# Performance work log

Measured on AMD Instinct MI355X. Metric: run time of the kernel, lower is better.

## Reference

```python
import jax, jax.numpy as jnp
import numpy as np

LN_EPS = 1e-5
LOCAL_SIZE = 256
N_HEAD, D_HEAD = 16, 64


def layer_norm_c(x):
    # layer norm over channel dim (axis=1), no affine params (matches F.layer_norm(x.T,(d,)).T)
    m = jnp.mean(x, axis=1, keepdims=True)
    v = jnp.var(x, axis=1, keepdims=True)
    return (x - m) / jnp.sqrt(v + LN_EPS)


def rel_shift(x):
    # x: [b, n, q, k] -> Transformer-XL relative shift
    b, n, q, k = x.shape
    x = jnp.pad(x, ((0, 0), (0, 0), (0, 0), (1, 0)))
    return x.reshape(b, n, k + 1, q)[:, :, 1:].reshape(b, n, q, k)


def setup_inputs() -> dict:
    key = jax.random.key(0)
    ks = jax.random.split(key, 14)
    bsz, d_model, qlen, mlen = 4, 1024, 512, 512
    klen = qlen + mlen
    d_inner = 4096
    s = lambda k, shape, sc=0.05: jax.random.normal(k, shape, dtype=jnp.float32) * sc
    return {
        "z1ss": jax.random.normal(ks[0], (bsz, d_model, qlen), dtype=jnp.float32),
        "uss": jax.random.normal(ks[1], (bsz, 3 * d_model, klen), dtype=jnp.float32) * 0.1,
        "z0": jax.random.normal(ks[2], (bsz, d_model, mlen), dtype=jnp.float32),
        "pos_emb": jax.random.normal(ks[3], (1, d_model, klen), dtype=jnp.float32),
        "qkv_w": s(ks[4], (3 * d_model, d_model)),
        "r_w": s(ks[5], (d_model, d_model)),
        "r_w_bias": s(ks[6], (N_HEAD, D_HEAD)),
        "r_r_bias": s(ks[7], (N_HEAD, D_HEAD)),
        "o_w": s(ks[8], (d_model, d_model)),
        "o_b": s(ks[9], (d_model,)),
        "ff1_w": s(ks[10], (d_inner, d_model)),
        "ff1_b": s(ks[11], (d_inner,)),
        "ff2_w": s(ks[12], (d_model, d_inner)),
        "ff2_b": s(ks[13], (d_model,)),
    }


def reference(z1ss, uss, z0, pos_emb, qkv_w, r_w, r_w_bias, r_r_bias, o_w, o_b,
              ff1_w, ff1_b, ff2_w, ff2_b):
    bsz, d_model, qlen = z1ss.shape
    mlen = z0.shape[2]
    n_head, d_head = N_HEAD, D_HEAD
    scale = 1.0 / d_head ** 0.5

    # ---- self-attention (post-lnorm path) ----
    cat = jnp.concatenate([z0, z1ss], axis=-1)              # [b, d, klen]
    klen = cat.shape[2]
    w_heads = jnp.einsum('od,bdk->bok', qkv_w, cat) + uss   # [b, 3d, klen]
    r_head_k = jnp.einsum('od,dk->ok', r_w, pos_emb[0])     # [d, rlen]
    rlen = r_head_k.shape[1]

    w_head_q, w_head_k, w_head_v = jnp.split(w_heads, 3, axis=1)
    w_head_q = w_head_q[:, :, -qlen:]
    w_head_q = w_head_q.reshape(bsz, n_head, d_head, qlen)
    w_head_k = w_head_k.reshape(bsz, n_head, d_head, klen)
    w_head_v = w_head_v.reshape(bsz, n_head, d_head, klen)
    r_head_k = r_head_k.reshape(n_head, d_head, rlen)

    rw_q = w_head_q + r_w_bias[:, :, None]                  # [b,n,d,q]
    AC = jnp.einsum('bndi,bndj->bnij', rw_q, w_head_k)      # [b,n,q,k]
    rr_q = w_head_q + r_r_bias[:, :, None]
    BD = rel_shift(jnp.einsum('bndi,ndj->bnij', rr_q, r_head_k))
    attn_score = (AC + BD) * scale

    local_size = LOCAL_SIZE if LOCAL_SIZE else 1000
    i = jnp.arange(qlen)[:, None]
    j = jnp.arange(klen)[None, :]
    mask = (j > i + mlen) | (j <= i + mlen - local_size)    # causal + local window
    attn_score = jnp.where(mask[None, None], -jnp.inf, attn_score)

    attn_prob = jax.nn.softmax(attn_score, axis=-1)
    attn_vec = jnp.einsum('bnij,bndj->bndi', attn_prob, w_head_v)
    attn_vec = attn_vec.reshape(bsz, n_head * d_head, qlen)
    attn_out = jnp.einsum('od,bdq->boq', o_w, attn_vec) + o_b[None, :, None]
    x = layer_norm_c(attn_out + z1ss)                       # post-lnorm

    # ---- position-wise FF (weight-shared, post-lnorm) ----
    h = jax.nn.relu(jnp.einsum('id,bdq->biq', ff1_w, x) + ff1_b[None, :, None])
    out2 = jnp.einsum('di,biq->bdq', ff2_w, h) + ff2_b[None, :, None]
    return layer_norm_c(out2 + x)
```

## Files before the change

kernel.cpp:

```cpp
#include <hip/hip_runtime.h>
#include <hip/hip_bf16.h>

typedef unsigned short u16;
typedef __attribute__((ext_vector_type(8))) short s8v;
typedef __attribute__((ext_vector_type(4))) short s4v;
typedef __attribute__((ext_vector_type(4))) float f4v;

__device__ __forceinline__ float s2f(u16 s) {
    unsigned int u = ((unsigned int)s) << 16;
    return __builtin_bit_cast(float, u);
}
__device__ __forceinline__ u16 f2s(float f) {
    __hip_bfloat16 h = __float2bfloat16(f);
    return __builtin_bit_cast(u16, h);
}

__device__ __forceinline__ void gl2lds16(const u16* g, u16* l) {
    __builtin_amdgcn_global_load_lds((const __attribute__((address_space(1))) void*)g,
                                     (__attribute__((address_space(3))) void*)l, 16, 0, 0);
}

#define BSZ 4
#define DM 1024
#define QLEN 512
#define MLEN 512
#define KLEN 1024
#define DI 4096
#define NH 16
#define DH 64
#define WIN 256

__global__ __launch_bounds__(256) void conv_w5(
    const float* __restrict__ s0, const float* __restrict__ s1,
    const float* __restrict__ s2, const float* __restrict__ s3,
    const float* __restrict__ s4,
    u16* __restrict__ d0, u16* __restrict__ d1, u16* __restrict__ d2,
    u16* __restrict__ d3, u16* __restrict__ d4)
{
    const int e0 = 786432, e1 = e0 + 262144, e2 = e1 + 262144,
              e3 = e2 + 1048576, e4 = e3 + 1048576;
    int i = blockIdx.x * 256 + threadIdx.x;
    const float* s; u16* d; int off;
    if (i < e0)      { s = s0; d = d0; off = i; }
    else if (i < e1) { s = s1; d = d1; off = i - e0; }
    else if (i < e2) { s = s2; d = d2; off = i - e1; }
    else if (i < e3) { s = s3; d = d3; off = i - e2; }
    else if (i < e4) { s = s4; d = d4; off = i - e3; }
    else return;
    f4v v = *(const f4v*)&s[(size_t)off * 4];
    s4v o;
#pragma unroll
    for (int k = 0; k < 4; ++k) o[k] = (short)f2s(v[k]);
    *(s4v*)&d[(size_t)off * 4] = o;
}

__global__ __launch_bounds__(256) void trans_f2b(
    const float* __restrict__ src, long sS, int ldS, int colOff,
    u16* __restrict__ dst, long sD, int ldD, int rowOff)
{
    __shared__ float tile[32][33];
    int b = blockIdx.z;
    int t0 = blockIdx.x * 32, f0 = blockIdx.y * 32;
    int tx = threadIdx.x, ty = threadIdx.y;
#pragma unroll
    for (int p = 0; p < 4; ++p)
        tile[ty + 8 * p][tx] = src[(size_t)b * sS + (size_t)(f0 + ty + 8 * p) * ldS + colOff + t0 + tx];
    __syncthreads();
#pragma unroll
    for (int p = 0; p < 4; ++p)
        dst[(size_t)b * sD + (size_t)(rowOff + t0 + ty + 8 * p) * ldD + f0 + tx] = f2s(tile[tx][ty + 8 * p]);
}

__global__ __launch_bounds__(256) void trans_add(
    const float* __restrict__ src, u16* __restrict__ dst)
{
    __shared__ float tile[32][33];
    int b = blockIdx.z;
    int t0 = blockIdx.x * 32, f0 = blockIdx.y * 32;
    int tx = threadIdx.x, ty = threadIdx.y;
    const float* S = src + (size_t)b * 3072 * 1024;
    u16* D = dst + (size_t)b * 1024 * 3072;
#pragma unroll
    for (int p = 0; p < 4; ++p)
        tile[ty + 8 * p][tx] = S[(size_t)(f0 + ty + 8 * p) * 1024 + t0 + tx];
    __syncthreads();
#pragma unroll
    for (int p = 0; p < 4; ++p) {
        size_t o = (size_t)(t0 + ty + 8 * p) * 3072 + f0 + tx;
        D[o] = f2s(s2f(D[o]) + tile[tx][ty + 8 * p]);
    }
}

__global__ __launch_bounds__(256) void trans_b2f(
    const u16* __restrict__ src, long sS, int ldS,
    float* __restrict__ dst, long sD, int ldD)
{
    __shared__ float tile[32][33];
    int b = blockIdx.z;
    int t0 = blockIdx.x * 32, f0 = blockIdx.y * 32;
    int tx = threadIdx.x, ty = threadIdx.y;
#pragma unroll
    for (int p = 0; p < 4; ++p)
        tile[ty + 8 * p][tx] = s2f(src[(size_t)b * sS + (size_t)(f0 + ty + 8 * p) * ldS + t0 + tx]);
    __syncthreads();
#pragma unroll
    for (int p = 0; p < 4; ++p)
        dst[(size_t)b * sD + (size_t)(t0 + ty + 8 * p) * ldD + f0 + tx] = tile[tx][ty + 8 * p];
}

template<int BN, int SPLIT>
__global__ __launch_bounds__(256) void gemm_bt(
    const u16* __restrict__ A,
    const u16* __restrict__ B,
    u16* __restrict__ C,
    float* __restrict__ fOut,
    int M, int K,
    const float* __restrict__ bias,
    const float* __restrict__ uss,
    int relu,
    long pstride)
{
    constexpr int BM = 128, BK = 64;
    constexpr int MI = (BN == 128) ? 4 : 2;
    constexpr int NI = 4;
    const int n0 = blockIdx.x * BN, m0 = blockIdx.y * BM;
    const int Ks = K / SPLIT;
    const int kbeg = blockIdx.z * Ks;
    __shared__ __align__(16) u16 As[BM * BK];
    __shared__ __align__(16) u16 Bs[BN * BK];
    const int tid = threadIdx.x, lane = tid & 63, wv = tid >> 6;
    const int l15 = lane & 15, quad = lane >> 4;
    const int wm = (BN == 128) ? (wv >> 1) * 64 : wv * 32;
    const int wn = (BN == 128) ? (wv & 1) * 64 : 0;
    f4v acc[MI][NI] = {};
    for (int kk = kbeg; kk < kbeg + Ks; kk += BK) {
        __syncthreads();
#pragma unroll
        for (int p = 0; p < (BM * 8) / 256; ++p) {
            int c = p * 256 + tid, r = c >> 3, q = c & 7, qs = q ^ (r & 7);
            gl2lds16(&A[(size_t)(m0 + r) * K + kk + qs * 8], &As[c * 8]);
        }
#pragma unroll
        for (int p = 0; p < (BN * 8) / 256; ++p) {
            int c = p * 256 + tid, r = c >> 3, q = c & 7, qs = q ^ (r & 7);
            gl2lds16(&B[(size_t)(n0 + r) * K + kk + qs * 8], &Bs[c * 8]);
        }
        __syncthreads();
#pragma unroll
        for (int k0 = 0; k0 < BK; k0 += 32) {
            s8v af[MI], bf[NI];
#pragma unroll
            for (int mi = 0; mi < MI; ++mi) {
                int r = wm + mi * 16 + l15;
                af[mi] = *(const s8v*)&As[r * BK + ((((k0 >> 3) + quad) ^ (r & 7)) << 3)];
            }
#pragma unroll
            for (int ni = 0; ni < NI; ++ni) {
                int r = wn + ni * 16 + l15;
                bf[ni] = *(const s8v*)&Bs[r * BK + ((((k0 >> 3) + quad) ^ (r & 7)) << 3)];
            }
#pragma unroll
            for (int mi = 0; mi < MI; ++mi)
#pragma unroll
                for (int ni = 0; ni < NI; ++ni)
                    acc[mi][ni] = __builtin_amdgcn_mfma_f32_16x16x32_bf16(af[mi], bf[ni], acc[mi][ni], 0, 0, 0);
        }
    }
    if (SPLIT > 1) {
        float* base = fOut + (long)blockIdx.z * pstride;
#pragma unroll
        for (int mi = 0; mi < MI; ++mi) {
            int m = m0 + wm + mi * 16 + quad * 4;
#pragma unroll
            for (int ni = 0; ni < NI; ++ni) {
                int n = n0 + wn + ni * 16 + l15;
                *(f4v*)&base[(size_t)n * M + m] = acc[mi][ni];
            }
        }
    } else {
#pragma unroll
        for (int mi = 0; mi < MI; ++mi) {
            int m = m0 + wm + mi * 16 + quad * 4;
            float bv[4] = {0.f, 0.f, 0.f, 0.f};
            if (bias) {
#pragma unroll
                for (int r2 = 0; r2 < 4; ++r2) bv[r2] = bias[m + r2];
            }
#pragma unroll
            for (int ni = 0; ni < NI; ++ni) {
                int n = n0 + wn + ni * 16 + l15;
                float o[4];
#pragma unroll
                for (int r2 = 0; r2 < 4; ++r2) o[r2] = acc[mi][ni][r2] + bv[r2];
                if (uss) {
                    int b = n >> 10, t = n & 1023;
#pragma unroll
                    for (int r2 = 0; r2 < 4; ++r2)
                        o[r2] += uss[((size_t)b * 3072 + m + r2) * 1024 + t];
                }
                if (relu) {
#pragma unroll
                    for (int r2 = 0; r2 < 4; ++r2) o[r2] = fmaxf(o[r2], 0.f);
                }
                s4v st;
#pragma unroll
                for (int r2 = 0; r2 < 4; ++r2) st[r2] = (short)f2s(o[r2]);
                *(s4v*)&C[(size_t)n * M + m] = st;
            }
        }
    }
}

#define QT 16
#define KT 272
#define KROW 72
#define VROW 280
#define SROW 272
#define PROW 280
__global__ __launch_bounds__(256) void attn_mfma(
    const u16* __restrict__ WHT,
    const u16* __restrict__ RT,
    const float* __restrict__ rwb, const float* __restrict__ rrb,
    u16* __restrict__ avT)
{
    __shared__ __align__(16) u16  sKV[KT * KROW];
    __shared__ __align__(16) float sS[QT * SROW];
    __shared__ __align__(16) u16  sP[QT * PROW];

    const int qt = blockIdx.x, n = blockIdx.y, b = blockIdx.z;
    const int i0 = qt * QT, j0 = i0 + WIN + 1;
    const int tid = threadIdx.x, lane = tid & 63, wv = tid >> 6;
    const int l15 = lane & 15, quad = lane >> 4;
    const u16* W = WHT + (size_t)b * KLEN * (3 * DM);

    s8v qac[2], qbd[2];
    {
        int qrow = MLEN + i0 + l15;
#pragma unroll
        for (int kc = 0; kc < 2; ++kc) {
            int col = n * DH + kc * 32 + quad * 8;
            s8v qv = *(const s8v*)&W[(size_t)qrow * (3 * DM) + col];
            s8v a, c;
#pragma unroll
            for (int e = 0; e < 8; ++e) {
                float qf = s2f((u16)qv[e]);
                a[e] = (short)f2s(qf + rwb[col + e]);
                c[e] = (short)f2s(qf + rrb[col + e]);
            }
            qac[kc] = a; qbd[kc] = c;
        }
    }

    for (int t = tid; t < KT * 8; t += 256) {
        int r = t >> 3, q = t & 7;
        int j = j0 + r; if (j > KLEN - 1) j = KLEN - 1;
        *(s8v*)&sKV[r * KROW + q * 8] = *(const s8v*)&W[(size_t)j * (3 * DM) + DM + n * DH + q * 8];
    }
    for (int t = tid; t < QT * SROW; t += 256) sS[t] = -1e30f;
    __syncthreads();

#pragma unroll
    for (int cc = 0; cc < 4; ++cc) {
        int ci = wv + cc * 4;
        f4v acc = {};
#pragma unroll
        for (int kc = 0; kc < 2; ++kc) {
            s8v bf = *(const s8v*)&RT[(size_t)(ci * 16 + l15) * DM + n * DH + kc * 32 + quad * 8];
            acc = __builtin_amdgcn_mfma_f32_16x16x32_bf16(qbd[kc], bf, acc, 0, 0, 0);
        }
#pragma unroll
        for (int r2 = 0; r2 < 4; ++r2) {
            int qi = quad * 4 + r2;
            sS[qi * SROW + qi + ci * 16 + l15] = acc[r2];
        }
    }
    __syncthreads();

    for (int ci = wv; ci < 17; ci += 4) {
        f4v acc = {};
#pragma unroll
        for (int kc = 0; kc < 2; ++kc) {
            s8v bf = *(const s8v*)&sKV[(ci * 16 + l15) * KROW + kc * 32 + quad * 8];
            acc = __builtin_amdgcn_mfma_f32_16x16x32_bf16(qac[kc], bf, acc, 0, 0, 0);
        }
#pragma unroll
        for (int r2 = 0; r2 < 4; ++r2) {
            int qi = quad * 4 + r2;
            sS[qi * SROW + ci * 16 + l15] += acc[r2];
        }
    }
    __syncthreads();

    {
        int q = tid >> 5, r0 = tid & 31;
        for (int k = 0; k < 9; ++k) {
            int r = r0 + 32 * k;
            if (r < KT) {
                int j = j0 + r; if (j > KLEN - 1) j = KLEN - 1;
                s8v vv = *(const s8v*)&W[(size_t)j * (3 * DM) + 2 * DM + n * DH + q * 8];
#pragma unroll
                for (int e = 0; e < 8; ++e)
                    sKV[(q * 8 + e) * VROW + r] = (u16)vv[e];
            }
        }
    }

    {
        int g = tid >> 4, l = tid & 15;
        float vals[17], mx = -1e30f;
#pragma unroll
        for (int k = 0; k < 17; ++k) {
            float s = sS[g * SROW + l + 16 * k] * 0.125f;
            vals[k] = s; mx = fmaxf(mx, s);
        }
#pragma unroll
        for (int d = 1; d < 16; d <<= 1) mx = fmaxf(mx, __shfl_xor(mx, d, 16));
        float sum = 0.f;
#pragma unroll
        for (int k = 0; k < 17; ++k) { vals[k] = __expf(vals[k] - mx); sum += vals[k]; }
#pragma unroll
        for (int d = 1; d < 16; d <<= 1) sum += __shfl_xor(sum, d, 16);
        float inv = 1.f / sum;
#pragma unroll
        for (int k = 0; k < 17; ++k) sP[g * PROW + l + 16 * k] = f2s(vals[k] * inv);
    }
    __syncthreads();

    f4v o = {};
    for (int kc = 0; kc < 9; ++kc) {
        s8v a = {}, bb = {};
        if (kc < 8) {
            a  = *(const s8v*)&sP[l15 * PROW + kc * 32 + quad * 8];
            bb = *(const s8v*)&sKV[(wv * 16 + l15) * VROW + kc * 32 + quad * 8];
        } else if (quad < 2) {
            a  = *(const s8v*)&sP[l15 * PROW + 256 + quad * 8];
            bb = *(const s8v*)&sKV[(wv * 16 + l15) * VROW + 256 + quad * 8];
        }
        o = __builtin_amdgcn_mfma_f32_16x16x32_bf16(a, bb, o, 0, 0, 0);
    }
#pragma unroll
    for (int r2 = 0; r2 < 4; ++r2) {
        int qi = quad * 4 + r2;
        avT[((size_t)b * QLEN + i0 + qi) * DM + n * DH + wv * 16 + l15] = f2s(o[r2]);
    }
}

__global__ __launch_bounds__(256) void ln_f(
    const float* __restrict__ P, long pstride, int nparts,
    const float* __restrict__ bias,
    const u16* __restrict__ res, int resMode, u16* __restrict__ out)
{
    int n = blockIdx.x, tid = threadIdx.x;
    int lane = tid & 63, wv = tid >> 6;
    int f = tid * 4;
    int rrow = resMode ? (((n >> 9) * 2 + 1) * 512 + (n & 511)) : n;
    f4v pv = *(const f4v*)&P[(size_t)n * DM + f];
    for (int p = 1; p < nparts; ++p) {
        const float* Pp = P + (long)p * pstride;
        pv += *(const f4v*)&Pp[(size_t)n * DM + f];
    }
    s4v rv = *(const s4v*)&res[(size_t)rrow * DM + f];
    f4v bv = *(const f4v*)&bias[f];
    float v[4];
#pragma unroll
    for (int k = 0; k < 4; ++k) v[k] = pv[k] + bv[k] + s2f((u16)rv[k]);
    float s = v[0] + v[1] + v[2] + v[3];
    float ss = v[0] * v[0] + v[1] * v[1] + v[2] * v[2] + v[3] * v[3];
#pragma unroll
    for (int d = 1; d < 64; d <<= 1) {
        s += __shfl_xor(s, d, 64);
        ss += __shfl_xor(ss, d, 64);
    }
    __shared__ float ps[4], pss[4];
    if (lane == 0) { ps[wv] = s; pss[wv] = ss; }
    __syncthreads();
    float S = ps[0] + ps[1] + ps[2] + ps[3];
    float SS = pss[0] + pss[1] + pss[2] + pss[3];
    float m = S * (1.f / DM);
    float var = SS * (1.f / DM) - m * m;
    float inv = rsqrtf(fmaxf(var, 0.f) + 1e-5f);
    s4v st;
#pragma unroll
    for (int k = 0; k < 4; ++k) st[k] = (short)f2s((v[k] - m) * inv);
    *(s4v*)&out[(size_t)n * DM + f] = st;
}

extern "C" void kernel_launch(void* const* d_in, const int* in_sizes, int n_in,
                              void* d_out, int out_size, void* d_ws, size_t ws_size,
                              hipStream_t stream) {
    const float* z1ss  = (const float*)d_in[0];
    const float* uss   = (const float*)d_in[1];
    const float* z0    = (const float*)d_in[2];
    const float* pos   = (const float*)d_in[3];
    const float* qkv_w = (const float*)d_in[4];
    const float* r_w   = (const float*)d_in[5];
    const float* rwb   = (const float*)d_in[6];
    const float* rrb   = (const float*)d_in[7];
    const float* o_w   = (const float*)d_in[8];
    const float* o_b   = (const float*)d_in[9];
    const float* ff1_w = (const float*)d_in[10];
    const float* ff1_b = (const float*)d_in[11];
    const float* ff2_w = (const float*)d_in[12];
    const float* ff2_b = (const float*)d_in[13];

    u16* ws = (u16*)d_ws;
    u16* wQ   = ws;
    u16* wR   = ws + 3145728;
    u16* wO   = ws + 4194304;
    u16* wF1  = ws + 5242880;
    u16* wF2  = ws + 9437184;
    u16* catT = ws + 13631488;
    u16* whT  = ws + 17825792;
    u16* posT = ws + 30408704;
    u16* rT   = ws + 30670848;
    u16* avT  = ws + 30932992;
    u16* xT   = ws + 33030144;
    float* pref = (float*)(ws + 35127296);
    u16* hT   = whT;
    u16* outT = catT;

    float* part1 = (float*)d_ws;
    long pstr = part1 - pref;

    dim3 tblk(32, 8);

    conv_w5<<<13312, 256, 0, stream>>>(qkv_w, r_w, o_w, ff1_w, ff2_w,
                                       wQ, wR, wO, wF1, wF2);

    trans_f2b<<<dim3(16, 32, BSZ), tblk, 0, stream>>>(z0, (long)DM * MLEN, MLEN, 0,
                                                      catT, (long)KLEN * DM, DM, 0);
    trans_f2b<<<dim3(16, 32, BSZ), tblk, 0, stream>>>(z1ss, (long)DM * QLEN, QLEN, 0,
                                                      catT, (long)KLEN * DM, DM, MLEN);
    trans_f2b<<<dim3(8, 32, 1), tblk, 0, stream>>>(pos, 0, KLEN, KLEN - WIN,
                                                   posT, 0, DM, 0);

    gemm_bt<64, 1><<<dim3(64, 24, 1), 256, 0, stream>>>(
        wQ, catT, whT, nullptr, 3 * DM, DM, nullptr, nullptr, 0, 0);

    trans_add<<<dim3(32, 96, BSZ), tblk, 0, stream>>>(uss, whT);

    gemm_bt<64, 1><<<dim3(4, 8, 1), 256, 0, stream>>>(
        wR, posT, rT, nullptr, DM, DM, nullptr, nullptr, 0, 0);

    attn_mfma<<<dim3(QLEN / QT, NH, BSZ), 256, 0, stream>>>(whT, rT, rwb, rrb, avT);

    gemm_bt<64, 2><<<dim3(32, 8, 2), 256, 0, stream>>>(
        wO, avT, nullptr, pref, DM, DM, nullptr, nullptr, 0, pstr);

    ln_f<<<2048, 256, 0, stream>>>(pref, pstr, 2, o_b, catT, 1, xT);

    gemm_bt<64, 1><<<dim3(32, 32, 1), 256, 0, stream>>>(
        wF1, xT, hT, nullptr, DI, DM, ff1_b, nullptr, 1, 0);

    gemm_bt<64, 2><<<dim3(32, 8, 2), 256, 0, stream>>>(
        wF2, hT, nullptr, pref, DM, DI, nullptr, nullptr, 0, pstr);

    ln_f<<<2048, 256, 0, stream>>>(pref, pstr, 2, ff2_b, xT, 0, outT);

    trans_b2f<<<dim3(32, 16, BSZ), tblk, 0, stream>>>(outT, (long)QLEN * DM, DM,
                                                      (float*)d_out, (long)DM * QLEN, QLEN);
}
```

Baseline: 365.1 us.

## Emit transposed V from QKV GEMM and stream K/V directly in attention

The QKV GEMM epilogue now adds uss to the V rows and writes V transposed (feature-major) into a separate buffer, so the transpose-add kernel only processes Q and K. The attention kernel drops its shared-memory K and V staging. It reads K and V fragments straight from global memory and applies the relative shift when storing scores, which cuts the score buffer to 256 columns. Probabilities are packed as bf16 into the score buffer, shared memory use shrinks, and launch bounds request 4 blocks per CU for more occupancy. The cost is scattered uncoalesced 2-byte stores in the GEMM epilogue and more uncached global loads in attention.

```diff
diff --git a/kernel.cpp b/kernel.cpp
--- a/kernel.cpp
+++ b/kernel.cpp
@@ -116,9 +116,10 @@
     float* __restrict__ fOut,
     int M, int K,
     const float* __restrict__ bias,
-    const float* __restrict__ uss,
     int relu,
-    long pstride)
+    long pstride,
+    const float* __restrict__ ussV,
+    u16* __restrict__ vTout)
 {
     constexpr int BM = 128, BK = 64;
     constexpr int MI = (BN == 128) ? 4 : 2;
@@ -177,6 +178,21 @@
                 *(f4v*)&base[(size_t)n * M + m] = acc[mi][ni];
             }
         }
+    } else if (vTout && m0 >= 2048) {
+#pragma unroll
+        for (int mi = 0; mi < MI; ++mi) {
+            int m = m0 + wm + mi * 16 + quad * 4;
+#pragma unroll
+            for (int ni = 0; ni < NI; ++ni) {
+                int n = n0 + wn + ni * 16 + l15;
+                int b = n >> 10, t = n & 1023;
+#pragma unroll
+                for (int r2 = 0; r2 < 4; ++r2) {
+                    float o = acc[mi][ni][r2] + ussV[((size_t)b * 3072 + (m + r2)) * 1024 + t];
+                    vTout[(size_t)(m + r2 - 2048) * 4096 + n] = f2s(o);
+                }
+            }
+        }
     } else {
 #pragma unroll
         for (int mi = 0; mi < MI; ++mi) {
@@ -192,12 +208,6 @@
                 float o[4];
 #pragma unroll
                 for (int r2 = 0; r2 < 4; ++r2) o[r2] = acc[mi][ni][r2] + bv[r2];
-                if (uss) {
-                    int b = n >> 10, t = n & 1023;
-#pragma unroll
-                    for (int r2 = 0; r2 < 4; ++r2)
-                        o[r2] += uss[((size_t)b * 3072 + m + r2) * 1024 + t];
-                }
                 if (relu) {
 #pragma unroll
                     for (int r2 = 0; r2 < 4; ++r2) o[r2] = fmaxf(o[r2], 0.f);
@@ -212,20 +222,15 @@
 }
 
 #define QT 16
-#define KT 272
-#define KROW 72
-#define VROW 280
-#define SROW 272
-#define PROW 280
-__global__ __launch_bounds__(256) void attn_mfma(
+#define SROW 260
+__global__ __launch_bounds__(256, 4) void attn_mfma(
     const u16* __restrict__ WHT,
+    const u16* __restrict__ VT,
     const u16* __restrict__ RT,
     const float* __restrict__ rwb, const float* __restrict__ rrb,
     u16* __restrict__ avT)
 {
-    __shared__ __align__(16) u16  sKV[KT * KROW];
     __shared__ __align__(16) float sS[QT * SROW];
-    __shared__ __align__(16) u16  sP[QT * PROW];
 
     const int qt = blockIdx.x, n = blockIdx.y, b = blockIdx.z;
     const int i0 = qt * QT, j0 = i0 + WIN + 1;
@@ -251,38 +256,27 @@
         }
     }
 
-    for (int t = tid; t < KT * 8; t += 256) {
-        int r = t >> 3, q = t & 7;
-        int j = j0 + r; if (j > KLEN - 1) j = KLEN - 1;
-        *(s8v*)&sKV[r * KROW + q * 8] = *(const s8v*)&W[(size_t)j * (3 * DM) + DM + n * DH + q * 8];
-    }
-    for (int t = tid; t < QT * SROW; t += 256) sS[t] = -1e30f;
+    for (int ci = wv; ci < 17; ci += 4) {
+        f4v acc = {};
+        const u16* Kr = &W[(size_t)(j0 + ci * 16 + l15) * (3 * DM) + DM + n * DH + quad * 8];
+        acc = __builtin_amdgcn_mfma_f32_16x16x32_bf16(qac[0], *(const s8v*)Kr, acc, 0, 0, 0);
+        acc = __builtin_amdgcn_mfma_f32_16x16x32_bf16(qac[1], *(const s8v*)(Kr + 32), acc, 0, 0, 0);
+#pragma unroll
+        for (int r2 = 0; r2 < 4; ++r2) {
+            int qi = quad * 4 + r2;
+            int t = ci * 16 + l15 - qi;
+            if ((unsigned)t < 256u) sS[qi * SROW + t] = acc[r2];
+        }
+    }
     __syncthreads();
 
 #pragma unroll
     for (int cc = 0; cc < 4; ++cc) {
         int ci = wv + cc * 4;
         f4v acc = {};
-#pragma unroll
-        for (int kc = 0; kc < 2; ++kc) {
-            s8v bf = *(const s8v*)&RT[(size_t)(ci * 16 + l15) * DM + n * DH + kc * 32 + quad * 8];
-            acc = __builtin_amdgcn_mfma_f32_16x16x32_bf16(qbd[kc], bf, acc, 0, 0, 0);
-        }
-#pragma unroll
-        for (int r2 = 0; r2 < 4; ++r2) {
-            int qi = quad * 4 + r2;
-            sS[qi * SROW + qi + ci * 16 + l15] = acc[r2];
-        }
-    }
-    __syncthreads();
-
-    for (int ci = wv; ci < 17; ci += 4) {
-        f4v acc = {};
-#pragma unroll
-        for (int kc = 0; kc < 2; ++kc) {
-            s8v bf = *(const s8v*)&sKV[(ci * 16 + l15) * KROW + kc * 32 + quad * 8];
-            acc = __builtin_amdgcn_mfma_f32_16x16x32_bf16(qac[kc], bf, acc, 0, 0, 0);
-        }
+        const u16* Rr = &RT[(size_t)(ci * 16 + l15) * DM + n * DH + quad * 8];
+        acc = __builtin_amdgcn_mfma_f32_16x16x32_bf16(qbd[0], *(const s8v*)Rr, acc, 0, 0, 0);
+        acc = __builtin_amdgcn_mfma_f32_16x16x32_bf16(qbd[1], *(const s8v*)(Rr + 32), acc, 0, 0, 0);
 #pragma unroll
         for (int r2 = 0; r2 < 4; ++r2) {
             int qi = quad * 4 + r2;
@@ -292,50 +286,40 @@
     __syncthreads();
 
     {
-        int q = tid >> 5, r0 = tid & 31;
-        for (int k = 0; k < 9; ++k) {
-            int r = r0 + 32 * k;
-            if (r < KT) {
-                int j = j0 + r; if (j > KLEN - 1) j = KLEN - 1;
-                s8v vv = *(const s8v*)&W[(size_t)j * (3 * DM) + 2 * DM + n * DH + q * 8];
-#pragma unroll
-                for (int e = 0; e < 8; ++e)
-                    sKV[(q * 8 + e) * VROW + r] = (u16)vv[e];
-            }
-        }
-    }
-
-    {
         int g = tid >> 4, l = tid & 15;
-        float vals[17], mx = -1e30f;
-#pragma unroll
-        for (int k = 0; k < 17; ++k) {
+        float vals[16], mx = -1e30f;
+#pragma unroll
+        for (int k = 0; k < 16; ++k) {
             float s = sS[g * SROW + l + 16 * k] * 0.125f;
             vals[k] = s; mx = fmaxf(mx, s);
         }
+        asm volatile("" ::: "memory");
 #pragma unroll
         for (int d = 1; d < 16; d <<= 1) mx = fmaxf(mx, __shfl_xor(mx, d, 16));
         float sum = 0.f;
 #pragma unroll
-        for (int k = 0; k < 17; ++k) { vals[k] = __expf(vals[k] - mx); sum += vals[k]; }
+        for (int k = 0; k < 16; ++k) { vals[k] = __expf(vals[k] - mx); sum += vals[k]; }
 #pragma unroll
         for (int d = 1; d < 16; d <<= 1) sum += __shfl_xor(sum, d, 16);
         float inv = 1.f / sum;
-#pragma unroll
-        for (int k = 0; k < 17; ++k) sP[g * PROW + l + 16 * k] = f2s(vals[k] * inv);
-    }
-    __syncthreads();
-
+        u16* sPr = (u16*)&sS[g * SROW];
+#pragma unroll
+        for (int k = 0; k < 16; ++k) sPr[g + 1 + l + 16 * k] = f2s(vals[k] * inv);
+        sPr[l <= g ? l : 256 + l] = 0;
+        sPr[272 + l] = 0;
+    }
+    __syncthreads();
+
+    const u16* sPu = (const u16*)sS;
+    const size_t vbase = (size_t)(n * DH + wv * 16 + l15) * 4096
+                       + (size_t)b * KLEN + (j0 - 1) + quad * 8;
     f4v o = {};
+#pragma unroll
     for (int kc = 0; kc < 9; ++kc) {
-        s8v a = {}, bb = {};
-        if (kc < 8) {
-            a  = *(const s8v*)&sP[l15 * PROW + kc * 32 + quad * 8];
-            bb = *(const s8v*)&sKV[(wv * 16 + l15) * VROW + kc * 32 + quad * 8];
-        } else if (quad < 2) {
-            a  = *(const s8v*)&sP[l15 * PROW + 256 + quad * 8];
-            bb = *(const s8v*)&sKV[(wv * 16 + l15) * VROW + 256 + quad * 8];
-        }
+        size_t vi = vbase + kc * 32;
+        if (vi > (size_t)4194304 - 8) vi = (size_t)4194304 - 8;
+        s8v a  = *(const s8v*)&sPu[(size_t)l15 * (2 * SROW) + kc * 32 + quad * 8];
+        s8v bb = *(const s8v*)&VT[vi];
         o = __builtin_amdgcn_mfma_f32_16x16x32_bf16(a, bb, o, 0, 0, 0);
     }
 #pragma unroll
@@ -419,6 +403,8 @@
     u16* hT   = whT;
     u16* outT = catT;
 
+    u16* vT = (u16*)pref;
+
     float* part1 = (float*)d_ws;
     long pstr = part1 - pref;
 
@@ -435,25 +421,25 @@
                                                    posT, 0, DM, 0);
 
     gemm_bt<64, 1><<<dim3(64, 24, 1), 256, 0, stream>>>(
-        wQ, catT, whT, nullptr, 3 * DM, DM, nullptr, nullptr, 0, 0);
-
-    trans_add<<<dim3(32, 96, BSZ), tblk, 0, stream>>>(uss, whT);
+        wQ, catT, whT, nullptr, 3 * DM, DM, nullptr, 0, 0, uss, vT);
+
+    trans_add<<<dim3(32, 64, BSZ), tblk, 0, stream>>>(uss, whT);
 
     gemm_bt<64, 1><<<dim3(4, 8, 1), 256, 0, stream>>>(
-        wR, posT, rT, nullptr, DM, DM, nullptr, nullptr, 0, 0);
-
-    attn_mfma<<<dim3(QLEN / QT, NH, BSZ), 256, 0, stream>>>(whT, rT, rwb, rrb, avT);
+        wR, posT, rT, nullptr, DM, DM, nullptr, 0, 0, nullptr, nullptr);
+
+    attn_mfma<<<dim3(QLEN / QT, NH, BSZ), 256, 0, stream>>>(whT, vT, rT, rwb, rrb, avT);
 
     gemm_bt<64, 2><<<dim3(32, 8, 2), 256, 0, stream>>>(
-        wO, avT, nullptr, pref, DM, DM, nullptr, nullptr, 0, pstr);
+        wO, avT, nullptr, pref, DM, DM, nullptr, 0, pstr, nullptr, nullptr);
 
     ln_f<<<2048, 256, 0, stream>>>(pref, pstr, 2, o_b, catT, 1, xT);
 
     gemm_bt<64, 1><<<dim3(32, 32, 1), 256, 0, stream>>>(
-        wF1, xT, hT, nullptr, DI, DM, ff1_b, nullptr, 1, 0);
+        wF1, xT, hT, nullptr, DI, DM, ff1_b, 1, 0, nullptr, nullptr);
 
     gemm_bt<64, 2><<<dim3(32, 8, 2), 256, 0, stream>>>(
-        wF2, hT, nullptr, pref, DM, DI, nullptr, nullptr, 0, pstr);
+        wF2, hT, nullptr, pref, DM, DI, nullptr, 0, pstr, nullptr, nullptr);
 
     ln_f<<<2048, 256, 0, stream>>>(pref, pstr, 2, ff2_b, xT, 0, outT);
 
```

Result: faster. 344.9 us (-5.5%).
